# Optimization experiments

Hardware: AMD Instinct MI355X
Metric: run time of the kernel (lower is better)

The kernel has to match this reference:

```python
import jax, jax.numpy as jnp
import numpy as np

B, N, K, F = 1, 50000, 16, 128
EPS = 1e-5

def _bn(h, gamma, beta):
    # BatchNorm1d in training mode: per-feature-channel stats over (batch, nodes)
    mean = jnp.mean(h, axis=(0, 1), keepdims=True)
    var = jnp.var(h, axis=(0, 1), keepdims=True)
    return (h - mean) * jax.lax.rsqrt(var + EPS) * gamma + beta

def _rgcn(h, neighbors, W, b):
    # pad one zero node row, gather K neighbors per node, flatten, linear
    h_pad = jnp.pad(h, ((0, 0), (0, 1), (0, 0)))           # [B, N+1, F]
    gathered = h_pad[:, neighbors]                          # [B, N, K, F]
    flat = gathered.reshape(h.shape[0], neighbors.shape[0], -1)  # [B, N, K*F]
    return jnp.einsum('bnk,ok->bno', flat, W) + b

def setup_inputs():
    key = jax.random.key(0)
    ks = jax.random.split(key, 10)
    x = jax.random.normal(ks[0], (B, N, F), jnp.float32)
    graph = jax.random.randint(ks[1], (N, K, 2), 0, N)
    gamma1 = 1.0 + 0.1 * jax.random.normal(ks[2], (F,), jnp.float32)
    beta1 = 0.1 * jax.random.normal(ks[3], (F,), jnp.float32)
    gamma2 = 1.0 + 0.1 * jax.random.normal(ks[4], (F,), jnp.float32)
    beta2 = 0.1 * jax.random.normal(ks[5], (F,), jnp.float32)
    s = 1.0 / np.sqrt(K * F)
    W1 = jax.random.uniform(ks[6], (F, K * F), jnp.float32, -s, s)
    b1 = jax.random.uniform(ks[7], (F,), jnp.float32, -s, s)
    W2 = jax.random.uniform(ks[8], (F, K * F), jnp.float32, -s, s)
    b2 = jax.random.uniform(ks[9], (F,), jnp.float32, -s, s)
    return {"x": x, "graph": graph, "gamma1": gamma1, "beta1": beta1,
            "W1": W1, "b1": b1, "gamma2": gamma2, "beta2": beta2,
            "W2": W2, "b2": b2}

def reference(x, graph, gamma1, beta1, W1, b1, gamma2, beta2, W2, b2):
    neighbors = graph[..., 1]                               # [N, K]
    out = jax.nn.gelu(_bn(x, gamma1, beta1), approximate=False)
    out = _rgcn(out, neighbors, W1, b1)                     # [B, N, F]
    out = jax.nn.gelu(_bn(out, gamma2, beta2), approximate=False)
    out = _rgcn(out, neighbors, W2, b2)                     # [B, N, F]
    return out + x
```

## Files before the change

### kernel.cpp

```cpp
#include <hip/hip_runtime.h>


#define NN 50000
#define FF 128

typedef __bf16 v8bf __attribute__((ext_vector_type(8)));
typedef float  v4f  __attribute__((ext_vector_type(4)));

__device__ __forceinline__ unsigned short f2bf(float f) {
  unsigned int u = __builtin_bit_cast(unsigned int, f);
  u += 0x7FFFu + ((u >> 16) & 1u);
  return (unsigned short)(u >> 16);
}
__device__ __forceinline__ float bf2f(unsigned short s) {
  unsigned int u = ((unsigned int)s) << 16;
  return __builtin_bit_cast(float, u);
}
__device__ __forceinline__ float gelu_f(float y) {
  return 0.5f * y * (1.0f + erff(y * 0.70710678118654752f));
}

__global__ void wconv_kernel(const float* __restrict__ W1, const float* __restrict__ W2,
                             unsigned short* __restrict__ Wt1, unsigned short* __restrict__ Wt2) {
  int t = blockIdx.x * 256 + threadIdx.x;
  const float* W = (t >= 32768) ? W2 : W1;
  unsigned short* Wt = (t >= 32768) ? Wt2 : Wt1;
  int r = t & 32767;
  int frag = r >> 6, lane = r & 63;
  int k4 = frag >> 3, c = frag & 7;
  int o  = c * 16 + (lane & 15);
  int kd = k4 * 32 + (lane >> 4) * 8;
  const float* src = W + o * 2048 + kd;
  unsigned short* dst = Wt + r * 8;
#pragma unroll
  for (int j = 0; j < 8; ++j) dst[j] = f2bf(src[j]);
}

__global__ void bn_stats_kernel(const float* __restrict__ x, float* __restrict__ part) {
  float s0=0,s1=0,s2=0,s3=0,q0=0,q1=0,q2=0,q3=0;
  for (int cb = blockIdx.x; cb < (NN*FF/1024); cb += 256) {
    float4 v = reinterpret_cast<const float4*>(x)[cb * 256 + threadIdx.x];
    s0+=v.x; q0+=v.x*v.x; s1+=v.y; q1+=v.y*v.y;
    s2+=v.z; q2+=v.z*v.z; s3+=v.w; q3+=v.w*v.w;
  }
  __shared__ float ls[1024], lsq[1024];
  int fb = (threadIdx.x & 31) * 4;
  int sl = threadIdx.x >> 5;
  ls[sl*128+fb]   = s0; ls[sl*128+fb+1]  = s1; ls[sl*128+fb+2]  = s2; ls[sl*128+fb+3]  = s3;
  lsq[sl*128+fb]  = q0; lsq[sl*128+fb+1] = q1; lsq[sl*128+fb+2] = q2; lsq[sl*128+fb+3] = q3;
  __syncthreads();
  if (threadIdx.x < 128) {
    float S=0,Q=0;
#pragma unroll
    for (int s2i=0; s2i<8; ++s2i){ S += ls[s2i*128+threadIdx.x]; Q += lsq[s2i*128+threadIdx.x]; }
    part[blockIdx.x*256 + threadIdx.x]       = S;
    part[blockIdx.x*256 + 128 + threadIdx.x] = Q;
  }
}

__global__ __launch_bounds__(1024) void bn_reduce_kernel(
    const float* __restrict__ part, int nb,
    const float* __restrict__ gamma, const float* __restrict__ beta,
    float* __restrict__ scsh) {
  int f = threadIdx.x & 127;
  int g = threadIdx.x >> 7;
  float S = 0.f, Q = 0.f;
  for (int b = g; b < nb; b += 8) {
    S += part[b * 256 + f];
    Q += part[b * 256 + 128 + f];
  }
  __shared__ float ls[8][128], lq[8][128];
  ls[g][f] = S; lq[g][f] = Q;
  __syncthreads();
  if (threadIdx.x < 128) {
    float St = 0.f, Qt = 0.f;
#pragma unroll
    for (int i = 0; i < 8; ++i) { St += ls[i][f]; Qt += lq[i][f]; }
    float inv  = 1.0f / (float)NN;
    float mean = St * inv;
    float var  = fmaxf(Qt * inv - mean * mean, 0.0f);
    float sc   = gamma[f] * rsqrtf(var + 1e-5f);
    scsh[f]       = sc;
    scsh[128 + f] = beta[f] - mean * sc;
  }
}

__global__ void apply1_kernel(const float* __restrict__ x, const float* __restrict__ scsh,
                              unsigned short* __restrict__ h1) {
  int stride = gridDim.x * blockDim.x;
  for (int c = blockIdx.x * blockDim.x + threadIdx.x; c < NN*FF/4; c += stride) {
    float4 v = reinterpret_cast<const float4*>(x)[c];
    int f = (c * 4) & 127;
    ushort4 o;
    o.x = f2bf(gelu_f(v.x * scsh[f]   + scsh[128+f]));
    o.y = f2bf(gelu_f(v.y * scsh[f+1] + scsh[128+f+1]));
    o.z = f2bf(gelu_f(v.z * scsh[f+2] + scsh[128+f+2]));
    o.w = f2bf(gelu_f(v.w * scsh[f+3] + scsh[128+f+3]));
    reinterpret_cast<ushort4*>(h1)[c] = o;
  }
}

__global__ void apply2_kernel(const unsigned short* __restrict__ t1, const float* __restrict__ scsh,
                              unsigned short* __restrict__ h2) {
  int stride = gridDim.x * blockDim.x;
  for (int c = blockIdx.x * blockDim.x + threadIdx.x; c < NN*FF/4; c += stride) {
    ushort4 v = reinterpret_cast<const ushort4*>(t1)[c];
    int f = (c * 4) & 127;
    ushort4 o;
    o.x = f2bf(gelu_f(bf2f(v.x) * scsh[f]   + scsh[128+f]));
    o.y = f2bf(gelu_f(bf2f(v.y) * scsh[f+1] + scsh[128+f+1]));
    o.z = f2bf(gelu_f(bf2f(v.z) * scsh[f+2] + scsh[128+f+2]));
    o.w = f2bf(gelu_f(bf2f(v.w) * scsh[f+3] + scsh[128+f+3]));
    reinterpret_cast<ushort4*>(h2)[c] = o;
  }
}

template<bool STATS>
__global__ __launch_bounds__(256, 2) void rgcn_kernel(
    const unsigned short* __restrict__ h,
    const unsigned short* __restrict__ Wt,
    const int* __restrict__ graph,
    const float* __restrict__ bias,
    const float* __restrict__ xres,
    float* __restrict__ outf,
    unsigned short* __restrict__ outb,
    float* __restrict__ part)
{
  __shared__ unsigned short bsm[2][16384];
  __shared__ float lds_s[4][128];
  __shared__ float lds_q[4][128];

  const int tid  = threadIdx.x;
  const int wv   = tid >> 6;
  const int lane = tid & 63;
  const int l15  = lane & 15;
  const int lq   = lane >> 4;
  const int nodebase = blockIdx.x * 128 + wv * 32;

  v4f acc[2][8];
#pragma unroll
  for (int rf = 0; rf < 2; ++rf)
#pragma unroll
    for (int c = 0; c < 8; ++c) acc[rf][c] = (v4f){0.f, 0.f, 0.f, 0.f};

  const int an0 = min(nodebase + l15, NN - 1);
  const int an1 = min(nodebase + 16 + l15, NN - 1);

  int idx0[16], idx1[16];
  {
    const int4* g0 = reinterpret_cast<const int4*>(graph + an0 * 32);
    const int4* g1 = reinterpret_cast<const int4*>(graph + an1 * 32);
#pragma unroll
    for (int j = 0; j < 8; ++j) {
      int4 t0 = g0[j], t1v = g1[j];
      idx0[2*j]   = min(max(t0.y,  0), NN - 1) * 128;
      idx0[2*j+1] = min(max(t0.w,  0), NN - 1) * 128;
      idx1[2*j]   = min(max(t1v.y, 0), NN - 1) * 128;
      idx1[2*j+1] = min(max(t1v.w, 0), NN - 1) * 128;
    }
  }

  v8bf A0[2][4], A1[2][4];
#define LOADA(buf_, s_) {                                             \
    const unsigned short* r0 = h + idx0[s_] + lq * 8;                 \
    const unsigned short* r1 = h + idx1[s_] + lq * 8;                 \
    _Pragma("unroll")                                                 \
    for (int w4 = 0; w4 < 4; ++w4) {                                  \
      A0[buf_][w4] = *reinterpret_cast<const v8bf*>(r0 + w4 * 32);    \
      A1[buf_][w4] = *reinterpret_cast<const v8bf*>(r1 + w4 * 32);    \
    }                                                                 \
  }

#define STAGE(buf_, s_) {                                                     \
    const unsigned short* gsrc = Wt + (s_) * 16384 + wv * 4096 + lane * 8;    \
    unsigned short* ldst = &bsm[buf_][wv * 4096];                             \
    _Pragma("unroll")                                                         \
    for (int i = 0; i < 8; ++i) {                                             \
      __builtin_amdgcn_global_load_lds(                                       \
        (const __attribute__((address_space(1))) void*)(gsrc + i * 512),      \
        (__attribute__((address_space(3))) void*)(ldst + i * 512),            \
        16, 0, 0);                                                            \
    }                                                                         \
  }

  STAGE(0, 0)
  LOADA(0, 0)
  __syncthreads();

#pragma unroll
  for (int s = 0; s < 16; ++s) {
    const int cur = s & 1, nxt = cur ^ 1;
    if (s < 15) {
      LOADA(nxt, s + 1)
      STAGE(nxt, s + 1)
    }
    __builtin_amdgcn_sched_barrier(0);
#pragma unroll
    for (int w4 = 0; w4 < 4; ++w4) {
#pragma unroll
      for (int c = 0; c < 8; ++c) {
        v8bf b = *reinterpret_cast<const v8bf*>(&bsm[cur][(w4 * 8 + c) * 512 + lane * 8]);
        acc[0][c] = __builtin_amdgcn_mfma_f32_16x16x32_bf16(A0[cur][w4], b, acc[0][c], 0, 0, 0);
        acc[1][c] = __builtin_amdgcn_mfma_f32_16x16x32_bf16(A1[cur][w4], b, acc[1][c], 0, 0, 0);
      }
    }
    __syncthreads();
  }
#undef LOADA
#undef STAGE

  if constexpr (STATS) {
#pragma unroll
    for (int c = 0; c < 8; ++c) {
      float s = 0.f, q = 0.f;
#pragma unroll
      for (int rf = 0; rf < 2; ++rf) {
#pragma unroll
        for (int j = 0; j < 4; ++j) {
          int node = nodebase + rf * 16 + lq * 4 + j;
          float v  = acc[rf][c][j];
          if (node < NN) {
            s += v; q += v * v;
            outb[node * 128 + c * 16 + l15] = f2bf(v);
          }
        }
      }
      s += __shfl_xor(s, 16, 64); s += __shfl_xor(s, 32, 64);
      q += __shfl_xor(q, 16, 64); q += __shfl_xor(q, 32, 64);
      if (lq == 0) { lds_s[wv][c * 16 + l15] = s; lds_q[wv][c * 16 + l15] = q; }
    }
    __syncthreads();
    if (tid < 128) {
      float S = lds_s[0][tid] + lds_s[1][tid] + lds_s[2][tid] + lds_s[3][tid];
      float Q = lds_q[0][tid] + lds_q[1][tid] + lds_q[2][tid] + lds_q[3][tid];
      part[blockIdx.x * 256 + tid]       = S;
      part[blockIdx.x * 256 + 128 + tid] = Q;
    }
  } else {
#pragma unroll
    for (int c = 0; c < 8; ++c) {
      float bv = bias[c * 16 + l15];
#pragma unroll
      for (int rf = 0; rf < 2; ++rf) {
#pragma unroll
        for (int j = 0; j < 4; ++j) {
          int node = nodebase + rf * 16 + lq * 4 + j;
          if (node < NN) {
            int idx = node * 128 + c * 16 + l15;
            outf[idx] = acc[rf][c][j] + bv + xres[idx];
          }
        }
      }
    }
  }
}

extern "C" void kernel_launch(void* const* d_in, const int* in_sizes, int n_in,
                              void* d_out, int out_size, void* d_ws, size_t ws_size,
                              hipStream_t stream) {
  const float* x      = (const float*)d_in[0];
  const int*   graph  = (const int*)d_in[1];
  const float* gamma1 = (const float*)d_in[2];
  const float* beta1  = (const float*)d_in[3];
  const float* W1     = (const float*)d_in[4];
  const float* gamma2 = (const float*)d_in[6];
  const float* beta2  = (const float*)d_in[7];
  const float* W2     = (const float*)d_in[8];
  const float* b2     = (const float*)d_in[9];
  float* out = (float*)d_out;

  char* ws = (char*)d_ws;
  unsigned short* h1  = (unsigned short*)(ws);
  unsigned short* t1  = (unsigned short*)(ws + 12800000);
  unsigned short* Wt1 = (unsigned short*)(ws + 25600000);
  unsigned short* Wt2 = (unsigned short*)(ws + 26124288);
  float* p1    = (float*)(ws + 26648576);
  float* p2    = (float*)(ws + 26910720);
  float* scsh1 = (float*)(ws + 27311104);
  float* scsh2 = (float*)(ws + 27312128);

  wconv_kernel<<<256, 256, 0, stream>>>(W1, W2, Wt1, Wt2);
  bn_stats_kernel<<<256, 256, 0, stream>>>(x, p1);
  bn_reduce_kernel<<<1, 1024, 0, stream>>>(p1, 256, gamma1, beta1, scsh1);
  apply1_kernel<<<2048, 256, 0, stream>>>(x, scsh1, h1);
  rgcn_kernel<true><<<391, 256, 0, stream>>>(h1, Wt1, graph, nullptr, nullptr, nullptr, t1, p2);
  bn_reduce_kernel<<<1, 1024, 0, stream>>>(p2, 391, gamma2, beta2, scsh2);
  apply2_kernel<<<2048, 256, 0, stream>>>(t1, scsh2, h1);
  rgcn_kernel<false><<<391, 256, 0, stream>>>(h1, Wt2, graph, b2, x, out, nullptr, nullptr);
}
```

Measured before the change: 207.7 us.

## Use partial vmcnt waits and raw barriers to overlap next-stage loads with MFMA

Replaces the loop's __syncthreads (which drains all outstanding memory ops) with explicit s_waitcnt vmcnt(16) followed by s_barrier. This lets the next stage's gather and LDS-staging loads stay in flight while the current stage's MFMAs run. The aim is to hide global/LDS load latency behind compute. It relies on the hand-counted vmcnt value matching the number of issued loads; if that count is wrong, the kernel reads incomplete data.

```diff
diff --git a/kernel.cpp b/kernel.cpp
--- a/kernel.cpp
+++ b/kernel.cpp
@@ -127,8 +127,6 @@
     float* __restrict__ part)
 {
   __shared__ unsigned short bsm[2][16384];
-  __shared__ float lds_s[4][128];
-  __shared__ float lds_q[4][128];
 
   const int tid  = threadIdx.x;
   const int wv   = tid >> 6;
@@ -183,33 +181,51 @@
     }                                                                         \
   }
 
+#define SLOT(s_) {                                                            \
+    if ((s_) < 15) {                                                          \
+      LOADA(((s_) + 1) & 1, (s_) + 1)                                         \
+      STAGE(((s_) + 1) & 1, (s_) + 1)                                         \
+    }                                                                         \
+    __builtin_amdgcn_sched_barrier(0);                                        \
+    if ((s_) < 15) { asm volatile("s_waitcnt vmcnt(16)" ::: "memory"); }      \
+    else           { asm volatile("s_waitcnt vmcnt(0)"  ::: "memory"); }      \
+    __builtin_amdgcn_sched_barrier(0);                                        \
+    __builtin_amdgcn_s_barrier();          \
+    __builtin_amdgcn_sched_barrier(0);                                        \
+    {                                                                         \
+      const int cur_ = (s_) & 1;                                              \
+      _Pragma("unroll")                                                       \
+      for (int w4 = 0; w4 < 4; ++w4) {                                        \
+        _Pragma("unroll")                                                     \
+        for (int c = 0; c < 8; ++c) {                                         \
+          v8bf b = *reinterpret_cast<const v8bf*>(                            \
+              &bsm[cur_][(w4 * 8 + c) * 512 + lane * 8]);                     \
+          acc[0][c] = __builtin_amdgcn_mfma_f32_16x16x32_bf16(                \
+                        A0[cur_][w4], b, acc[0][c], 0, 0, 0);                 \
+          acc[1][c] = __builtin_amdgcn_mfma_f32_16x16x32_bf16(                \
+                        A1[cur_][w4], b, acc[1][c], 0, 0, 0);                 \
+        }                                                                     \
+      }                                                                       \
+    }                                                                         \
+    __builtin_amdgcn_sched_barrier(0);                                        \
+    __builtin_amdgcn_s_barrier();      \
+    __builtin_amdgcn_sched_barrier(0);                                        \
+  }
+
   STAGE(0, 0)
   LOADA(0, 0)
-  __syncthreads();
-
-#pragma unroll
-  for (int s = 0; s < 16; ++s) {
-    const int cur = s & 1, nxt = cur ^ 1;
-    if (s < 15) {
-      LOADA(nxt, s + 1)
-      STAGE(nxt, s + 1)
-    }
-    __builtin_amdgcn_sched_barrier(0);
-#pragma unroll
-    for (int w4 = 0; w4 < 4; ++w4) {
-#pragma unroll
-      for (int c = 0; c < 8; ++c) {
-        v8bf b = *reinterpret_cast<const v8bf*>(&bsm[cur][(w4 * 8 + c) * 512 + lane * 8]);
-        acc[0][c] = __builtin_amdgcn_mfma_f32_16x16x32_bf16(A0[cur][w4], b, acc[0][c], 0, 0, 0);
-        acc[1][c] = __builtin_amdgcn_mfma_f32_16x16x32_bf16(A1[cur][w4], b, acc[1][c], 0, 0, 0);
-      }
-    }
-    __syncthreads();
-  }
+
+  SLOT(0)  SLOT(1)  SLOT(2)  SLOT(3)
+  SLOT(4)  SLOT(5)  SLOT(6)  SLOT(7)
+  SLOT(8)  SLOT(9)  SLOT(10) SLOT(11)
+  SLOT(12) SLOT(13) SLOT(14) SLOT(15)
+#undef SLOT
 #undef LOADA
 #undef STAGE
 
   if constexpr (STATS) {
+    __shared__ float lds_s[4][128];
+    __shared__ float lds_q[4][128];
 #pragma unroll
     for (int c = 0; c < 8; ++c) {
       float s = 0.f, q = 0.f;
```

After: 205.4 us. No clear change (-1.1%).
